# Kernel optimization log

Hardware: AMD Instinct MI355X
Metric: run time of the kernel (lower is better)

## Reference

```python
import jax, jax.numpy as jnp
import numpy as np

N, E = 20000, 320000
EPS = 1e-5
NEG_SLOPE = 0.2


def gat_conv(x, src, dst, W, att_src, att_dst, bias, num_nodes):
    # W: [Fin, H*C], att_*: [H, C], bias: [H*C]
    H, C = att_src.shape
    h = (x @ W).reshape(num_nodes, H, C)            # [N,H,C]
    a_s = jnp.einsum('nhc,hc->nh', h, att_src)      # [N,H]
    a_d = jnp.einsum('nhc,hc->nh', h, att_dst)      # [N,H]
    e = jax.nn.leaky_relu(a_s[src] + a_d[dst], NEG_SLOPE)  # [E,H]
    m = jax.ops.segment_max(e, dst, num_segments=num_nodes)       # per-dst max (self-loops guarantee non-empty)
    ex = jnp.exp(e - m[dst])
    s = jax.ops.segment_sum(ex, dst, num_segments=num_nodes)
    alpha = ex / s[dst]                              # [E,H] segment softmax
    out = jax.ops.segment_sum(h[src] * alpha[:, :, None], dst, num_segments=num_nodes)  # [N,H,C]
    return out.reshape(num_nodes, H * C) + bias


def batch_norm(x, gamma, beta):
    mu = x.mean(axis=0)
    var = x.var(axis=0)  # biased, as torch BN uses for normalization
    return (x - mu) * jax.lax.rsqrt(var + EPS) * gamma + beta


def setup_inputs() -> dict:
    key = jax.random.key(0)
    ks = jax.random.split(key, 32)
    x = jax.random.normal(ks[0], (N, 512), dtype=jnp.float32)
    edge_index = jax.random.randint(ks[1], (2, E), 0, N, dtype=jnp.int32)
    d = {"x": x, "edge_index": edge_index}
    # layer configs: (Fin, C_out, H)
    cfgs = [(512, 64, 8), (512, 64, 4), (256, 64, 2), (128, 16, 1)]
    i = 2
    for li, (fin, c, h) in enumerate(cfgs, start=1):
        sc = 1.0 / np.sqrt(fin)
        d[f"W{li}"] = jax.random.normal(ks[i], (fin, h * c), dtype=jnp.float32) * sc; i += 1
        d[f"as{li}"] = jax.random.normal(ks[i], (h, c), dtype=jnp.float32) * 0.1; i += 1
        d[f"ad{li}"] = jax.random.normal(ks[i], (h, c), dtype=jnp.float32) * 0.1; i += 1
        d[f"b{li}"] = jnp.zeros((h * c,), dtype=jnp.float32)
        if li < 4:
            d[f"g{li}"] = jnp.ones((h * c,), dtype=jnp.float32)
            d[f"be{li}"] = jnp.zeros((h * c,), dtype=jnp.float32)
    return d


def reference(x, edge_index, W1, as1, ad1, b1, g1, be1, W2, as2, ad2, b2, g2, be2, W3, as3, ad3, b3, g3, be3, W4, as4, ad4, b4):
    num_nodes = x.shape[0]
    loop = jnp.arange(num_nodes, dtype=edge_index.dtype)
    src = jnp.concatenate([edge_index[0], loop])  # add_self_loops=True
    dst = jnp.concatenate([edge_index[1], loop])
    h = gat_conv(x, src, dst, W1, as1, ad1, b1, num_nodes)
    h = jax.nn.elu(batch_norm(h, g1, be1))
    h = gat_conv(h, src, dst, W2, as2, ad2, b2, num_nodes)
    h = jax.nn.elu(batch_norm(h, g2, be2))
    h = gat_conv(h, src, dst, W3, as3, ad3, b3, num_nodes)
    h = jax.nn.elu(batch_norm(h, g3, be3))
    h = gat_conv(h, src, dst, W4, as4, ad4, b4, num_nodes)
    return jax.nn.log_softmax(h, axis=1)
```

## Files before the change

kernel.cpp:

```cpp
#include <hip/hip_runtime.h>
#include <hip/hip_bf16.h>
#include <cstdint>
#include <cstddef>

#define NN 20000
#define EE 320000
#define ET (EE + NN)
#define MPAD 20096
#define BNP 256
#define SCHUNK 20

typedef __attribute__((ext_vector_type(8))) short  short8;
typedef __attribute__((ext_vector_type(4))) float  floatx4;

__device__ inline unsigned short f2bf(float f) {
    unsigned u = __float_as_uint(f);
    u += 0x7FFFu + ((u >> 16) & 1u);
    return (unsigned short)(u >> 16);
}
__device__ inline float bf2f(unsigned short b) {
    return __uint_as_float(((unsigned)b) << 16);
}
__device__ inline float bflo(unsigned u) { return __uint_as_float(u << 16); }
__device__ inline float bfhi(unsigned u) { return __uint_as_float(u & 0xFFFF0000u); }

__global__ void zero_i32(int* __restrict__ p, int n) {
    int i = blockIdx.x * blockDim.x + threadIdx.x;
    if (i < n) p[i] = 0;
}

__global__ void cvt_a_bf16(const float* __restrict__ in, unsigned short* __restrict__ out,
                           int M, int Mpad, int K) {
    long long base = ((long long)blockIdx.x * blockDim.x + threadIdx.x) * 4;
    if (base >= (long long)Mpad * K) return;
    int row = (int)(base / K);
    float4 v = make_float4(0.f, 0.f, 0.f, 0.f);
    if (row < M) v = *(const float4*)(in + base);
    ushort4 o;
    o.x = f2bf(v.x); o.y = f2bf(v.y); o.z = f2bf(v.z); o.w = f2bf(v.w);
    *(ushort4*)(out + base) = o;
}

__global__ void cvt_w_t(const float* __restrict__ W, unsigned short* __restrict__ Wt,
                        int K, int N) {
    int i = blockIdx.x * blockDim.x + threadIdx.x;
    if (i >= K * N) return;
    int k = i / N, n = i - k * N;
    Wt[(size_t)n * K + k] = f2bf(W[i]);
}

__global__ void count_edges(const int* __restrict__ dst, int* __restrict__ cnt) {
    int e = blockIdx.x * blockDim.x + threadIdx.x;
    if (e >= ET) return;
    int d = (e < EE) ? dst[e] : (e - EE);
    atomicAdd(&cnt[d], 1);
}

__global__ __launch_bounds__(1024) void scan_fast(const int* __restrict__ cnt,
                                                  int* __restrict__ rowp,
                                                  int* __restrict__ wptr, int n) {
    __shared__ int sums[1024];
    const int t = threadIdx.x;
    const int base = t * SCHUNK;
    int local[SCHUNK];
    int acc = 0;
#pragma unroll
    for (int i = 0; i < SCHUNK; ++i) {
        int idx = base + i;
        int v = (idx < n) ? cnt[idx] : 0;
        local[i] = acc;
        acc += v;
    }
    sums[t] = acc;
    __syncthreads();
    for (int o = 1; o < 1024; o <<= 1) {
        int u = (t >= o) ? sums[t - o] : 0;
        __syncthreads();
        sums[t] += u;
        __syncthreads();
    }
    int excl = sums[t] - acc;
#pragma unroll
    for (int i = 0; i < SCHUNK; ++i) {
        int idx = base + i;
        if (idx < n) { int rp = excl + local[i]; rowp[idx] = rp; wptr[idx] = rp; }
    }
    if (t == 1023) rowp[n] = sums[1023];
}

__global__ void fill_edges(const int* __restrict__ src, const int* __restrict__ dst,
                           int* __restrict__ wptr, int* __restrict__ colx) {
    int e = blockIdx.x * blockDim.x + threadIdx.x;
    if (e >= ET) return;
    int s, d;
    if (e < EE) { s = src[e]; d = dst[e]; } else { s = e - EE; d = e - EE; }
    int pos = atomicAdd(&wptr[d], 1);
    colx[pos] = s;
}

__global__ __launch_bounds__(256) void gemm_bf16_fused(
        const unsigned short* __restrict__ A, const unsigned short* __restrict__ Bt,
        unsigned short* __restrict__ hN, float* __restrict__ aS, float* __restrict__ aD,
        const float* __restrict__ atts, const float* __restrict__ attd,
        int M, int N, int K) {
    __shared__ unsigned short As[128][40];
    __shared__ unsigned short Bs[128][40];
    const int t = threadIdx.x;
    const int lane = t & 63, wave = t >> 6;
    const int wm = wave >> 1, wn = wave & 1;
    const int quad = lane >> 4, mrow = lane & 15;
    const int row0 = blockIdx.y * 128, col0 = blockIdx.x * 128;
    const int srow = t >> 2, schunk = (t & 3) * 8;

    floatx4 acc[4][4];
#pragma unroll
    for (int i = 0; i < 4; ++i)
#pragma unroll
        for (int j = 0; j < 4; ++j)
#pragma unroll
            for (int r = 0; r < 4; ++r) acc[i][j][r] = 0.f;

    for (int k0 = 0; k0 < K; k0 += 32) {
        uint4 ra0 = *(const uint4*)(A  + (size_t)(row0 + srow)      * K + k0 + schunk);
        uint4 ra1 = *(const uint4*)(A  + (size_t)(row0 + srow + 64) * K + k0 + schunk);
        uint4 rb0 = *(const uint4*)(Bt + (size_t)(col0 + srow)      * K + k0 + schunk);
        uint4 rb1 = *(const uint4*)(Bt + (size_t)(col0 + srow + 64) * K + k0 + schunk);
        __syncthreads();
        *(uint4*)&As[srow][schunk]      = ra0;
        *(uint4*)&As[srow + 64][schunk] = ra1;
        *(uint4*)&Bs[srow][schunk]      = rb0;
        *(uint4*)&Bs[srow + 64][schunk] = rb1;
        __syncthreads();

        short8 af[4], bfr[4];
#pragma unroll
        for (int i = 0; i < 4; ++i)
            af[i] = *(const short8*)&As[wm * 64 + i * 16 + mrow][quad * 8];
#pragma unroll
        for (int j = 0; j < 4; ++j)
            bfr[j] = *(const short8*)&Bs[wn * 64 + j * 16 + mrow][quad * 8];
#pragma unroll
        for (int i = 0; i < 4; ++i)
#pragma unroll
            for (int j = 0; j < 4; ++j)
                acc[i][j] = __builtin_amdgcn_mfma_f32_16x16x32_bf16(af[i], bfr[j], acc[i][j], 0, 0, 0);
    }

    const int head = (col0 + wn * 64) >> 6;
    float attS[4], attD[4];
#pragma unroll
    for (int j = 0; j < 4; ++j) {
        attS[j] = atts[head * 64 + j * 16 + mrow];
        attD[j] = attd[head * 64 + j * 16 + mrow];
    }

#pragma unroll
    for (int i = 0; i < 4; ++i) {
#pragma unroll
        for (int r = 0; r < 4; ++r) {
            int row = row0 + wm * 64 + i * 16 + quad * 4 + r;
            float ps = acc[i][0][r] * attS[0] + acc[i][1][r] * attS[1]
                     + acc[i][2][r] * attS[2] + acc[i][3][r] * attS[3];
            float pd = acc[i][0][r] * attD[0] + acc[i][1][r] * attD[1]
                     + acc[i][2][r] * attD[2] + acc[i][3][r] * attD[3];
#pragma unroll
            for (int o = 1; o < 16; o <<= 1) {
                ps += __shfl_xor(ps, o);
                pd += __shfl_xor(pd, o);
            }
            if (row < M) {
                if (mrow == 0) {
                    aS[(size_t)head * M + row] = ps;
                    aD[(size_t)head * M + row] = pd;
                }
#pragma unroll
                for (int j = 0; j < 4; ++j)
                    hN[(size_t)row * N + col0 + wn * 64 + j * 16 + mrow] = f2bf(acc[i][j][r]);
            }
        }
    }
}

template <int HH>
__global__ __launch_bounds__(256) void gat_agg_head16(
        const unsigned short* __restrict__ hN,
        const float* __restrict__ aS, const float* __restrict__ aD,
        const int* __restrict__ rowp, const int* __restrict__ colx,
        const float* __restrict__ bias, float* __restrict__ out, int Nn) {
    constexpr int F = HH * 64;
    constexpr int G = 8 / HH;
    __shared__ uint2 pair[4][4][17];
    const int L = blockIdx.x;
    const int x8 = L & 7;
    const int hd = x8 / G;
    const int nodeblk = (L >> 3) * G + (x8 & (G - 1));
    const int wave = threadIdx.x >> 6, lane = threadIdx.x & 63;
    const int grp = lane >> 4;
    const int q   = lane & 15;
    const int n = nodeblk * 16 + wave * 4 + grp;
    if (n >= Nn) return;

    const float* aSh = aS + (size_t)hd * Nn;
    const float adv = aD[(size_t)hd * Nn + n];
    const int b0 = rowp[n], b1 = rowp[n + 1];
    const unsigned short* hbase = hN + hd * 64;

    float m = -1e30f, s = 0.f;
    float a0 = 0.f, a1 = 0.f, a2 = 0.f, a3 = 0.f;

    for (int c0 = b0; c0 < b1; c0 += 16) {
        const int cnt = min(16, b1 - c0);
        int sn = 0; float e = -1e30f;
        if (q < cnt) {
            sn = colx[c0 + q];
            float tt = aSh[sn] + adv;
            e = (tt > 0.f) ? tt : 0.2f * tt;
        }
        float mc = e;
#pragma unroll
        for (int o = 8; o > 0; o >>= 1) mc = fmaxf(mc, __shfl_xor(mc, o));
        float nm = fmaxf(m, mc);
        float sc = __expf(m - nm);
        float p = (q < cnt) ? __expf(e - nm) : 0.f;
        float ps = p;
#pragma unroll
        for (int o = 8; o > 0; o >>= 1) ps += __shfl_xor(ps, o);
        s = s * sc + ps;
        a0 *= sc; a1 *= sc; a2 *= sc; a3 *= sc;
        m = nm;

        pair[wave][grp][q] = make_uint2((unsigned)sn, __float_as_uint(p));
        __threadfence_block();

        const int iters = (cnt + 3) >> 2;
        for (int it = 0; it < iters; ++it) {
            const int j = it << 2;
            uint2 e0 = pair[wave][grp][j + 0];
            uint2 e1 = pair[wave][grp][j + 1];
            uint2 e2 = pair[wave][grp][j + 2];
            uint2 e3 = pair[wave][grp][j + 3];
            uint2 v0 = *(const uint2*)(hbase + (size_t)e0.x * F + q * 4);
            uint2 v1 = *(const uint2*)(hbase + (size_t)e1.x * F + q * 4);
            uint2 v2 = *(const uint2*)(hbase + (size_t)e2.x * F + q * 4);
            uint2 v3 = *(const uint2*)(hbase + (size_t)e3.x * F + q * 4);
            float p0 = __uint_as_float(e0.y), p1 = __uint_as_float(e1.y);
            float p2 = __uint_as_float(e2.y), p3 = __uint_as_float(e3.y);
            a0 += p0 * bflo(v0.x) + p1 * bflo(v1.x) + p2 * bflo(v2.x) + p3 * bflo(v3.x);
            a1 += p0 * bfhi(v0.x) + p1 * bfhi(v1.x) + p2 * bfhi(v2.x) + p3 * bfhi(v3.x);
            a2 += p0 * bflo(v0.y) + p1 * bflo(v1.y) + p2 * bflo(v2.y) + p3 * bflo(v3.y);
            a3 += p0 * bfhi(v0.y) + p1 * bfhi(v1.y) + p2 * bfhi(v2.y) + p3 * bfhi(v3.y);
        }
        __threadfence_block();
    }

    const float inv = 1.f / s;
    const int cb = hd * 64 + q * 4;
    float4 o4;
    o4.x = a0 * inv + bias[cb + 0];
    o4.y = a1 * inv + bias[cb + 1];
    o4.z = a2 * inv + bias[cb + 2];
    o4.w = a3 * inv + bias[cb + 3];
    *(float4*)(out + (size_t)n * F + cb) = o4;
}

__global__ __launch_bounds__(256) void gemm_l4_fused(const unsigned short* __restrict__ A,
                                                     const float* __restrict__ B,
                                                     unsigned short* __restrict__ C,
                                                     float* __restrict__ aS, float* __restrict__ aD,
                                                     const float* __restrict__ atts,
                                                     const float* __restrict__ attd,
                                                     int M, int N, int K) {
    __shared__ float As[16][65];
    __shared__ float Bs[16][64];
    const int tid = threadIdx.x;
    const int tx = tid & 15, ty = tid >> 4;
    const int row0 = blockIdx.y * 64, col0 = blockIdx.x * 64;
    const int rA = tid >> 2, kq = (tid & 3) << 2;
    const int rB = tid >> 4, cq = (tid & 15) << 2;
    float acc[4][4] = {};

    for (int k0 = 0; k0 < K; k0 += 16) {
        ushort4 ha = *(const ushort4*)(A + (size_t)(row0 + rA) * K + k0 + kq);
        float4 fb = make_float4(0.f, 0.f, 0.f, 0.f);
        int bcol = col0 + cq;
        if (bcol < N) fb = *(const float4*)(B + (size_t)(k0 + rB) * N + bcol);
        As[kq + 0][rA] = bf2f(ha.x); As[kq + 1][rA] = bf2f(ha.y);
        As[kq + 2][rA] = bf2f(ha.z); As[kq + 3][rA] = bf2f(ha.w);
        *(float4*)&Bs[rB][cq] = fb;
        __syncthreads();
#pragma unroll
        for (int k = 0; k < 16; ++k) {
            float a0 = As[k][ty * 4 + 0];
            float a1 = As[k][ty * 4 + 1];
            float a2 = As[k][ty * 4 + 2];
            float a3 = As[k][ty * 4 + 3];
            float4 b = *(float4*)&Bs[k][tx * 4];
            acc[0][0] += a0 * b.x; acc[0][1] += a0 * b.y; acc[0][2] += a0 * b.z; acc[0][3] += a0 * b.w;
            acc[1][0] += a1 * b.x; acc[1][1] += a1 * b.y; acc[1][2] += a1 * b.z; acc[1][3] += a1 * b.w;
            acc[2][0] += a2 * b.x; acc[2][1] += a2 * b.y; acc[2][2] += a2 * b.z; acc[2][3] += a2 * b.w;
            acc[3][0] += a3 * b.x; acc[3][1] += a3 * b.y; acc[3][2] += a3 * b.z; acc[3][3] += a3 * b.w;
        }
        __syncthreads();
    }
    float as_part[4], ad_part[4];
#pragma unroll
    for (int i = 0; i < 4; ++i) { as_part[i] = 0.f; ad_part[i] = 0.f; }
    if (tx < 4) {
#pragma unroll
        for (int i = 0; i < 4; ++i) {
#pragma unroll
            for (int jj = 0; jj < 4; ++jj) {
                int c = tx * 4 + jj;
                as_part[i] += acc[i][jj] * atts[c];
                ad_part[i] += acc[i][jj] * attd[c];
            }
        }
    }
#pragma unroll
    for (int i = 0; i < 4; ++i) {
        float ps = as_part[i], pd = ad_part[i];
        ps += __shfl_xor(ps, 1); ps += __shfl_xor(ps, 2);
        pd += __shfl_xor(pd, 1); pd += __shfl_xor(pd, 2);
        int r = row0 + ty * 4 + i;
        if (r < M) {
            if (tx == 0) { aS[r] = ps; aD[r] = pd; }
#pragma unroll
            for (int jj = 0; jj < 4; ++jj) {
                int c = col0 + tx * 4 + jj;
                if (c < N) C[(size_t)r * N + c] = f2bf(acc[i][jj]);
            }
        }
    }
}

template <int C>
__global__ void gat_agg_l4_ls(const unsigned short* __restrict__ ht,
                              const float* __restrict__ as, const float* __restrict__ aD,
                              const int* __restrict__ rowp, const int* __restrict__ colx,
                              const float* __restrict__ bias, float* __restrict__ out, int Nn) {
    int n = blockIdx.x * 4 + (threadIdx.x >> 6);
    int lane = threadIdx.x & 63;
    if (n >= Nn) return;
    float adv = aD[n];
    int b0 = rowp[n], b1 = rowp[n + 1];

    float m = -1e30f, s = 0.f, acc = 0.f;
    for (int c0 = b0; c0 < b1; c0 += 64) {
        int cnt = b1 - c0; if (cnt > 64) cnt = 64;
        int sn = 0; float e = -1e30f;
        if (lane < cnt) {
            sn = colx[c0 + lane];
            float tt = as[sn] + adv;
            e = (tt > 0.f) ? tt : 0.2f * tt;
        }
        float mc = e;
#pragma unroll
        for (int o = 32; o > 0; o >>= 1) mc = fmaxf(mc, __shfl_xor(mc, o));
        float nm = fmaxf(m, mc);
        float sc = __expf(m - nm);
        acc *= sc; s *= sc;
        float p = (lane < cnt) ? __expf(e - nm) : 0.f;
        float ps = p;
#pragma unroll
        for (int o = 32; o > 0; o >>= 1) ps += __shfl_xor(ps, o);
        s += ps; m = nm;

        int j = 0;
        for (; j + 4 <= cnt; j += 4) {
            int s0 = __shfl(sn, j),     s1 = __shfl(sn, j + 1);
            int s2 = __shfl(sn, j + 2), s3 = __shfl(sn, j + 3);
            float p0 = __shfl(p, j),     p1 = __shfl(p, j + 1);
            float p2 = __shfl(p, j + 2), p3 = __shfl(p, j + 3);
            float h0 = 0.f, h1 = 0.f, h2 = 0.f, h3 = 0.f;
            if (lane < C) {
                h0 = bf2f(ht[(size_t)s0 * C + lane]);
                h1 = bf2f(ht[(size_t)s1 * C + lane]);
                h2 = bf2f(ht[(size_t)s2 * C + lane]);
                h3 = bf2f(ht[(size_t)s3 * C + lane]);
            }
            acc += p0 * h0 + p1 * h1 + p2 * h2 + p3 * h3;
        }
        for (; j < cnt; ++j) {
            int sj = __shfl(sn, j);
            float pj = __shfl(p, j);
            float hv = (lane < C) ? bf2f(ht[(size_t)sj * C + lane]) : 0.f;
            acc += pj * hv;
        }
    }
    float v = (lane < C) ? (acc / s + bias[lane]) : -1e30f;
    float mx = v;
#pragma unroll
    for (int o = 8; o > 0; o >>= 1) mx = fmaxf(mx, __shfl_xor(mx, o));
    float ex = (lane < C) ? __expf(v - mx) : 0.f;
#pragma unroll
    for (int o = 8; o > 0; o >>= 1) ex += __shfl_xor(ex, o);
    float l = __logf(ex) + mx;
    if (lane < C) out[(size_t)n * C + lane] = v - l;
}

template <int F>
__global__ __launch_bounds__(256) void bn_stats_det(const float* __restrict__ x,
                                                    float* __restrict__ part,
                                                    long long total) {
    constexpr int R  = 1024 / F;
    constexpr int NT = F / 4;
    __shared__ float sd[256 * 9];
    const int t = threadIdx.x;
    long long idx = ((long long)blockIdx.x * 256 + t) * 4;
    const long long stride = (long long)gridDim.x * 1024;
    float s0 = 0, s1 = 0, s2 = 0, s3 = 0, q0 = 0, q1 = 0, q2 = 0, q3 = 0;
    for (; idx < total; idx += stride) {
        float4 v = *(const float4*)(x + idx);
        s0 += v.x; q0 += v.x * v.x;
        s1 += v.y; q1 += v.y * v.y;
        s2 += v.z; q2 += v.z * v.z;
        s3 += v.w; q3 += v.w * v.w;
    }
    sd[t * 9 + 0] = s0; sd[t * 9 + 1] = s1; sd[t * 9 + 2] = s2; sd[t * 9 + 3] = s3;
    sd[t * 9 + 4] = q0; sd[t * 9 + 5] = q1; sd[t * 9 + 6] = q2; sd[t * 9 + 7] = q3;
    __syncthreads();
    if (t < NT) {
        float a[8];
#pragma unroll
        for (int k = 0; k < 8; ++k) a[k] = sd[t * 9 + k];
        for (int r = 1; r < R; ++r)
#pragma unroll
            for (int k = 0; k < 8; ++k) a[k] += sd[(t + r * NT) * 9 + k];
        int col = t * 4;
        float* pb = part + (size_t)blockIdx.x * 2 * F;
#pragma unroll
        for (int k = 0; k < 4; ++k) {
            pb[col + k]     = a[k];
            pb[F + col + k] = a[4 + k];
        }
    }
}

template <int F>
__global__ __launch_bounds__(256) void bn_reduce_par(const float* __restrict__ part,
                                                     const float* __restrict__ gamma,
                                                     const float* __restrict__ beta,
                                                     float* __restrict__ ss,
                                                     float invN) {
    __shared__ float sd[8][33];
    const int t = threadIdx.x;
    const int pr = t >> 5;
    const int tg = t & 31;
    const int c0 = blockIdx.x * 16;
    const int col = (tg < 16) ? (c0 + tg) : (F + c0 + (tg - 16));
    float a = 0.f;
    for (int p = pr; p < BNP; p += 8)
        a += part[(size_t)p * 2 * F + col];
    sd[pr][tg] = a;
    __syncthreads();
    if (pr == 0) {
        float tot = sd[0][tg];
#pragma unroll
        for (int r = 1; r < 8; ++r) tot += sd[r][tg];
        sd[0][tg] = tot;
    }
    __syncthreads();
    if (t < 16) {
        int c = c0 + t;
        float s = sd[0][t];
        float q = sd[0][16 + t];
        float mu = s * invN;
        float var = q * invN - mu * mu;
        float sc = gamma[c] * rsqrtf(var + 1e-5f);
        ss[c] = sc;
        ss[F + c] = beta[c] - mu * sc;
    }
}

__global__ void bn_apply_elu_bf16(const float* __restrict__ x, const float* __restrict__ ss,
                                  unsigned short* __restrict__ outA,
                                  int Nn, int F, int fmask) {
    long long idx4 = ((long long)blockIdx.x * blockDim.x + threadIdx.x) * 4;
    int row = (int)(idx4 / F);
    ushort4 o = make_ushort4(0, 0, 0, 0);
    if (row < Nn) {
        int c = (int)(idx4 & fmask);
        float4 v = *(const float4*)(x + idx4);
        float v0 = v.x * ss[c + 0] + ss[F + c + 0];
        float v1 = v.y * ss[c + 1] + ss[F + c + 1];
        float v2 = v.z * ss[c + 2] + ss[F + c + 2];
        float v3 = v.w * ss[c + 3] + ss[F + c + 3];
        v0 = (v0 > 0.f) ? v0 : (__expf(v0) - 1.f);
        v1 = (v1 > 0.f) ? v1 : (__expf(v1) - 1.f);
        v2 = (v2 > 0.f) ? v2 : (__expf(v2) - 1.f);
        v3 = (v3 > 0.f) ? v3 : (__expf(v3) - 1.f);
        o.x = f2bf(v0); o.y = f2bf(v1); o.z = f2bf(v2); o.w = f2bf(v3);
    }
    *(ushort4*)(outA + idx4) = o;
}

extern "C" void kernel_launch(void* const* d_in, const int* in_sizes, int n_in,
                              void* d_out, int out_size, void* d_ws, size_t ws_size,
                              hipStream_t stream) {
    const float* x   = (const float*)d_in[0];
    const int*   ei  = (const int*)d_in[1];
    const float* W1  = (const float*)d_in[2];
    const float* as1 = (const float*)d_in[3];
    const float* ad1 = (const float*)d_in[4];
    const float* b1  = (const float*)d_in[5];
    const float* ga1 = (const float*)d_in[6];
    const float* be1 = (const float*)d_in[7];
    const float* W2  = (const float*)d_in[8];
    const float* as2 = (const float*)d_in[9];
    const float* ad2 = (const float*)d_in[10];
    const float* b2  = (const float*)d_in[11];
    const float* ga2 = (const float*)d_in[12];
    const float* be2 = (const float*)d_in[13];
    const float* W3  = (const float*)d_in[14];
    const float* as3 = (const float*)d_in[15];
    const float* ad3 = (const float*)d_in[16];
    const float* b3  = (const float*)d_in[17];
    const float* ga3 = (const float*)d_in[18];
    const float* be3 = (const float*)d_in[19];
    const float* W4  = (const float*)d_in[20];
    const float* as4 = (const float*)d_in[21];
    const float* ad4 = (const float*)d_in[22];
    const float* b4  = (const float*)d_in[23];
    float* outp = (float*)d_out;

    uint8_t* base = (uint8_t*)d_ws;
    size_t off = 0;
    auto alloc = [&](size_t nbytes) -> void* {
        off = (off + 255) & ~(size_t)255;
        void* p = base + off;
        off += nbytes;
        return p;
    };
    float* bufO = (float*)alloc((size_t)NN * 512 * 4);
    unsigned short* bufA = (unsigned short*)alloc((size_t)MPAD * 512 * 2);
    unsigned short* hN   = (unsigned short*)alloc((size_t)NN * 512 * 2);
    unsigned short* Wt1  = (unsigned short*)alloc((size_t)512 * 512 * 2);
    unsigned short* Wt2  = (unsigned short*)alloc((size_t)256 * 512 * 2);
    unsigned short* Wt3  = (unsigned short*)alloc((size_t)128 * 256 * 2);
    float* aSn  = (float*)alloc((size_t)NN * 8 * 4);
    float* aDn  = (float*)alloc((size_t)NN * 8 * 4);
    int*   cnt  = (int*)alloc((size_t)NN * 4);
    int*   rowp = (int*)alloc((size_t)(NN + 1) * 4);
    int*   wptr = (int*)alloc((size_t)NN * 4);
    int*   colx = (int*)alloc((size_t)ET * 4);
    float* bnp  = (float*)alloc((size_t)BNP * 1024 * 4);
    float* bns  = (float*)alloc((size_t)1024 * 4);

    const int* srcRow = ei;
    const int* dstRow = ei + EE;

    zero_i32<<<(NN + 255) / 256, 256, 0, stream>>>(cnt, NN);
    count_edges<<<(ET + 255) / 256, 256, 0, stream>>>(dstRow, cnt);
    scan_fast<<<1, 1024, 0, stream>>>(cnt, rowp, wptr, NN);
    fill_edges<<<(ET + 255) / 256, 256, 0, stream>>>(srcRow, dstRow, wptr, colx);

    cvt_w_t<<<(512 * 512 + 255) / 256, 256, 0, stream>>>(W1, Wt1, 512, 512);
    cvt_w_t<<<(512 * 256 + 255) / 256, 256, 0, stream>>>(W2, Wt2, 512, 256);
    cvt_w_t<<<(256 * 128 + 255) / 256, 256, 0, stream>>>(W3, Wt3, 256, 128);

    const int NBLK = (NN + 15) / 16;

    {
        cvt_a_bf16<<<((MPAD * 512 / 4) + 255) / 256, 256, 0, stream>>>(x, bufA, NN, MPAD, 512);
        dim3 g(512 / 128, MPAD / 128);
        gemm_bf16_fused<<<g, 256, 0, stream>>>(bufA, Wt1, hN, aSn, aDn, as1, ad1, NN, 512, 512);
        gat_agg_head16<8><<<NBLK * 8, 256, 0, stream>>>(hN, aSn, aDn, rowp, colx, b1, bufO, NN);
        bn_stats_det<512><<<BNP, 256, 0, stream>>>(bufO, bnp, (long long)NN * 512);
        bn_reduce_par<512><<<512 / 16, 256, 0, stream>>>(bnp, ga1, be1, bns, 1.0f / NN);
        bn_apply_elu_bf16<<<(MPAD * 512 / 4) / 256, 256, 0, stream>>>(bufO, bns, bufA, NN, 512, 511);
    }
    {
        dim3 g(256 / 128, MPAD / 128);
        gemm_bf16_fused<<<g, 256, 0, stream>>>(bufA, Wt2, hN, aSn, aDn, as2, ad2, NN, 256, 512);
        gat_agg_head16<4><<<((NBLK + 1) / 2) * 8, 256, 0, stream>>>(hN, aSn, aDn, rowp, colx, b2, bufO, NN);
        bn_stats_det<256><<<BNP, 256, 0, stream>>>(bufO, bnp, (long long)NN * 256);
        bn_reduce_par<256><<<256 / 16, 256, 0, stream>>>(bnp, ga2, be2, bns, 1.0f / NN);
        bn_apply_elu_bf16<<<(MPAD * 256 / 4) / 256, 256, 0, stream>>>(bufO, bns, bufA, NN, 256, 255);
    }
    {
        dim3 g(128 / 128, MPAD / 128);
        gemm_bf16_fused<<<g, 256, 0, stream>>>(bufA, Wt3, hN, aSn, aDn, as3, ad3, NN, 128, 256);
        gat_agg_head16<2><<<((NBLK + 3) / 4) * 8, 256, 0, stream>>>(hN, aSn, aDn, rowp, colx, b3, bufO, NN);
        bn_stats_det<128><<<BNP, 256, 0, stream>>>(bufO, bnp, (long long)NN * 128);
        bn_reduce_par<128><<<128 / 16, 256, 0, stream>>>(bnp, ga3, be3, bns, 1.0f / NN);
        bn_apply_elu_bf16<<<(MPAD * 128 / 4) / 256, 256, 0, stream>>>(bufO, bns, bufA, NN, 128, 127);
    }
    {
        dim3 g(1, (NN + 63) / 64);
        gemm_l4_fused<<<g, 256, 0, stream>>>(bufA, W4, hN, aSn, aDn, as4, ad4, NN, 16, 128);
        gat_agg_l4_ls<16><<<(NN + 3) / 4, 256, 0, stream>>>(hN, aSn, aDn, rowp, colx, b4, outp, NN);
    }
}
```

Before: 451.5 us.

## Fuse BN reduce via last-block ticket, widen aggregation chunks, merge weight casts

Folds the BN partial-sum reduction into the stats kernel: a ticket atomic lets the last block reduce all partials and write scale/shift, which removes one launch per layer. The GAT aggregation now handles 32 neighbors per chunk, with two per lane, so there are fewer online-softmax rescale rounds for typical degree around 17. The three weight-transpose launches are merged into one. In exchange, the final reduction runs serially in a single block, and it depends on the tickets being zeroed by zero_i32 on every call.

```diff
diff --git a/kernel.cpp b/kernel.cpp
--- a/kernel.cpp
+++ b/kernel.cpp
@@ -41,12 +41,20 @@
     *(ushort4*)(out + base) = o;
 }
 
-__global__ void cvt_w_t(const float* __restrict__ W, unsigned short* __restrict__ Wt,
-                        int K, int N) {
+#define W1SZ (512 * 512)
+#define W2SZ (512 * 256)
+#define W3SZ (256 * 128)
+__global__ void cvt_w_all(const float* __restrict__ W1, unsigned short* __restrict__ Wt1,
+                          const float* __restrict__ W2, unsigned short* __restrict__ Wt2,
+                          const float* __restrict__ W3, unsigned short* __restrict__ Wt3) {
     int i = blockIdx.x * blockDim.x + threadIdx.x;
-    if (i >= K * N) return;
-    int k = i / N, n = i - k * N;
-    Wt[(size_t)n * K + k] = f2bf(W[i]);
+    const float* W; unsigned short* Wt; int K, N, idx;
+    if (i < W1SZ)               { W = W1; Wt = Wt1; K = 512; N = 512; idx = i; }
+    else if (i < W1SZ + W2SZ)   { W = W2; Wt = Wt2; K = 512; N = 256; idx = i - W1SZ; }
+    else if (i < W1SZ + W2SZ + W3SZ) { W = W3; Wt = Wt3; K = 256; N = 128; idx = i - W1SZ - W2SZ; }
+    else return;
+    int k = idx / N, n = idx - k * N;
+    Wt[(size_t)n * K + k] = f2bf(W[idx]);
 }
 
 __global__ void count_edges(const int* __restrict__ dst, int* __restrict__ cnt) {
@@ -182,14 +190,14 @@
 }
 
 template <int HH>
-__global__ __launch_bounds__(256) void gat_agg_head16(
+__global__ __launch_bounds__(256) void gat_agg_head32(
         const unsigned short* __restrict__ hN,
         const float* __restrict__ aS, const float* __restrict__ aD,
         const int* __restrict__ rowp, const int* __restrict__ colx,
         const float* __restrict__ bias, float* __restrict__ out, int Nn) {
     constexpr int F = HH * 64;
     constexpr int G = 8 / HH;
-    __shared__ uint2 pair[4][4][17];
+    __shared__ uint2 pair[4][4][33];
     const int L = blockIdx.x;
     const int x8 = L & 7;
     const int hd = x8 / G;
@@ -205,52 +213,82 @@
     const int b0 = rowp[n], b1 = rowp[n + 1];
     const unsigned short* hbase = hN + hd * 64;
 
-    float m = -1e30f, s = 0.f;
+    float m, s;
     float a0 = 0.f, a1 = 0.f, a2 = 0.f, a3 = 0.f;
 
-    for (int c0 = b0; c0 < b1; c0 += 16) {
-        const int cnt = min(16, b1 - c0);
-        int sn = 0; float e = -1e30f;
-        if (q < cnt) {
-            sn = colx[c0 + q];
-            float tt = aSh[sn] + adv;
-            e = (tt > 0.f) ? tt : 0.2f * tt;
-        }
-        float mc = e;
+    auto gather = [&](int cnt) {
+        const int iters = (cnt + 3) >> 2;
+        for (int it = 0; it < iters; ++it) {
+            const int j = it << 2;
+            uint2 x0 = pair[wave][grp][j + 0];
+            uint2 x1 = pair[wave][grp][j + 1];
+            uint2 x2 = pair[wave][grp][j + 2];
+            uint2 x3 = pair[wave][grp][j + 3];
+            uint2 v0 = *(const uint2*)(hbase + (size_t)x0.x * F + q * 4);
+            uint2 v1 = *(const uint2*)(hbase + (size_t)x1.x * F + q * 4);
+            uint2 v2 = *(const uint2*)(hbase + (size_t)x2.x * F + q * 4);
+            uint2 v3 = *(const uint2*)(hbase + (size_t)x3.x * F + q * 4);
+            float p0 = __uint_as_float(x0.y), p1 = __uint_as_float(x1.y);
+            float p2 = __uint_as_float(x2.y), p3 = __uint_as_float(x3.y);
+            a0 += p0 * bflo(v0.x) + p1 * bflo(v1.x) + p2 * bflo(v2.x) + p3 * bflo(v3.x);
+            a1 += p0 * bfhi(v0.x) + p1 * bfhi(v1.x) + p2 * bfhi(v2.x) + p3 * bfhi(v3.x);
+            a2 += p0 * bflo(v0.y) + p1 * bflo(v1.y) + p2 * bflo(v2.y) + p3 * bflo(v3.y);
+            a3 += p0 * bfhi(v0.y) + p1 * bfhi(v1.y) + p2 * bfhi(v2.y) + p3 * bfhi(v3.y);
+        }
+    };
+
+    {
+        const int cnt = min(32, b1 - b0);
+        int sn0 = 0, sn1 = 0;
+        if (q < cnt)      sn0 = colx[b0 + q];
+        if (q + 16 < cnt) sn1 = colx[b0 + q + 16];
+        float t0 = aSh[sn0] + adv;
+        float t1 = aSh[sn1] + adv;
+        float e0 = (q < cnt)      ? ((t0 > 0.f) ? t0 : 0.2f * t0) : -1e30f;
+        float e1 = (q + 16 < cnt) ? ((t1 > 0.f) ? t1 : 0.2f * t1) : -1e30f;
+        float mc = fmaxf(e0, e1);
+#pragma unroll
+        for (int o = 8; o > 0; o >>= 1) mc = fmaxf(mc, __shfl_xor(mc, o));
+        m = mc;
+        float p0 = __expf(e0 - m);
+        float p1 = __expf(e1 - m);
+        float ps = p0 + p1;
+#pragma unroll
+        for (int o = 8; o > 0; o >>= 1) ps += __shfl_xor(ps, o);
+        s = ps;
+        pair[wave][grp][q]      = make_uint2((unsigned)sn0, __float_as_uint(p0));
+        pair[wave][grp][q + 16] = make_uint2((unsigned)sn1, __float_as_uint(p1));
+        __threadfence_block();
+        gather(cnt);
+    }
+
+    for (int c0 = b0 + 32; c0 < b1; c0 += 32) {
+        __threadfence_block();
+        const int cnt = min(32, b1 - c0);
+        int sn0 = 0, sn1 = 0;
+        if (q < cnt)      sn0 = colx[c0 + q];
+        if (q + 16 < cnt) sn1 = colx[c0 + q + 16];
+        float t0 = aSh[sn0] + adv;
+        float t1 = aSh[sn1] + adv;
+        float e0 = (q < cnt)      ? ((t0 > 0.f) ? t0 : 0.2f * t0) : -1e30f;
+        float e1 = (q + 16 < cnt) ? ((t1 > 0.f) ? t1 : 0.2f * t1) : -1e30f;
+        float mc = fmaxf(e0, e1);
 #pragma unroll
         for (int o = 8; o > 0; o >>= 1) mc = fmaxf(mc, __shfl_xor(mc, o));
         float nm = fmaxf(m, mc);
         float sc = __expf(m - nm);
-        float p = (q < cnt) ? __expf(e - nm) : 0.f;
-        float ps = p;
+        float p0 = __expf(e0 - nm);
+        float p1 = __expf(e1 - nm);
+        float ps = p0 + p1;
 #pragma unroll
         for (int o = 8; o > 0; o >>= 1) ps += __shfl_xor(ps, o);
         s = s * sc + ps;
         a0 *= sc; a1 *= sc; a2 *= sc; a3 *= sc;
         m = nm;
-
-        pair[wave][grp][q] = make_uint2((unsigned)sn, __float_as_uint(p));
+        pair[wave][grp][q]      = make_uint2((unsigned)sn0, __float_as_uint(p0));
+        pair[wave][grp][q + 16] = make_uint2((unsigned)sn1, __float_as_uint(p1));
         __threadfence_block();
-
-        const int iters = (cnt + 3) >> 2;
-        for (int it = 0; it < iters; ++it) {
-            const int j = it << 2;
-            uint2 e0 = pair[wave][grp][j + 0];
-            uint2 e1 = pair[wave][grp][j + 1];
-            uint2 e2 = pair[wave][grp][j + 2];
-            uint2 e3 = pair[wave][grp][j + 3];
-            uint2 v0 = *(const uint2*)(hbase + (size_t)e0.x * F + q * 4);
-            uint2 v1 = *(const uint2*)(hbase + (size_t)e1.x * F + q * 4);
-            uint2 v2 = *(const uint2*)(hbase + (size_t)e2.x * F + q * 4);
-            uint2 v3 = *(const uint2*)(hbase + (size_t)e3.x * F + q * 4);
-            float p0 = __uint_as_float(e0.y), p1 = __uint_as_float(e1.y);
-            float p2 = __uint_as_float(e2.y), p3 = __uint_as_float(e3.y);
-            a0 += p0 * bflo(v0.x) + p1 * bflo(v1.x) + p2 * bflo(v2.x) + p3 * bflo(v3.x);
-            a1 += p0 * bfhi(v0.x) + p1 * bfhi(v1.x) + p2 * bfhi(v2.x) + p3 * bfhi(v3.x);
-            a2 += p0 * bflo(v0.y) + p1 * bflo(v1.y) + p2 * bflo(v2.y) + p3 * bflo(v3.y);
-            a3 += p0 * bfhi(v0.y) + p1 * bfhi(v1.y) + p2 * bfhi(v2.y) + p3 * bfhi(v3.y);
-        }
-        __threadfence_block();
+        gather(cnt);
     }
 
     const float inv = 1.f / s;
@@ -399,9 +437,11 @@
 }
 
 template <int F>
-__global__ __launch_bounds__(256) void bn_stats_det(const float* __restrict__ x,
-                                                    float* __restrict__ part,
-                                                    long long total) {
+__global__ __launch_bounds__(256) void bn_stats_fused(
+        const float* __restrict__ x, float* __restrict__ part,
+        const float* __restrict__ gamma, const float* __restrict__ beta,
+        float* __restrict__ ss, int* __restrict__ ticket,
+        long long total, float invN) {
     constexpr int R  = 1024 / F;
     constexpr int NT = F / 4;
     __shared__ float sd[256 * 9];
@@ -434,40 +474,26 @@
             pb[F + col + k] = a[4 + k];
         }
     }
-}
-
-template <int F>
-__global__ __launch_bounds__(256) void bn_reduce_par(const float* __restrict__ part,
-                                                     const float* __restrict__ gamma,
-                                                     const float* __restrict__ beta,
-                                                     float* __restrict__ ss,
-                                                     float invN) {
-    __shared__ float sd[8][33];
-    const int t = threadIdx.x;
-    const int pr = t >> 5;
-    const int tg = t & 31;
-    const int c0 = blockIdx.x * 16;
-    const int col = (tg < 16) ? (c0 + tg) : (F + c0 + (tg - 16));
-    float a = 0.f;
-    for (int p = pr; p < BNP; p += 8)
-        a += part[(size_t)p * 2 * F + col];
-    sd[pr][tg] = a;
+    __threadfence();
+    __shared__ int amLast;
+    if (t == 0) amLast = (atomicAdd(ticket, 1) == (int)gridDim.x - 1);
     __syncthreads();
-    if (pr == 0) {
-        float tot = sd[0][tg];
-#pragma unroll
-        for (int r = 1; r < 8; ++r) tot += sd[r][tg];
-        sd[0][tg] = tot;
+    if (!amLast) return;
+    __threadfence();
+    for (int col = t; col < 2 * F; col += 256) {
+        float a = 0.f;
+        for (int p = 0; p < BNP; ++p)
+            a += part[(size_t)p * 2 * F + col];
+        sd[col] = a;
     }
     __syncthreads();
-    if (t < 16) {
-        int c = c0 + t;
-        float s = sd[0][t];
-        float q = sd[0][16 + t];
-        float mu = s * invN;
-        float var = q * invN - mu * mu;
-        float sc = gamma[c] * rsqrtf(var + 1e-5f);
-        ss[c] = sc;
+    for (int c = t; c < F; c += 256) {
+        float sum = sd[c];
+        float sq  = sd[F + c];
+        float mu  = sum * invN;
+        float var = sq * invN - mu * mu;
+        float sc  = gamma[c] * rsqrtf(var + 1e-5f);
+        ss[c]     = sc;
         ss[F + c] = beta[c] - mu * sc;
     }
 }
@@ -539,24 +565,23 @@
     unsigned short* Wt3  = (unsigned short*)alloc((size_t)128 * 256 * 2);
     float* aSn  = (float*)alloc((size_t)NN * 8 * 4);
     float* aDn  = (float*)alloc((size_t)NN * 8 * 4);
-    int*   cnt  = (int*)alloc((size_t)NN * 4);
+    int*   cnt  = (int*)alloc((size_t)(NN + 64) * 4);
     int*   rowp = (int*)alloc((size_t)(NN + 1) * 4);
     int*   wptr = (int*)alloc((size_t)NN * 4);
     int*   colx = (int*)alloc((size_t)ET * 4);
     float* bnp  = (float*)alloc((size_t)BNP * 1024 * 4);
     float* bns  = (float*)alloc((size_t)1024 * 4);
+    int* tickets = cnt + NN;
 
     const int* srcRow = ei;
     const int* dstRow = ei + EE;
 
-    zero_i32<<<(NN + 255) / 256, 256, 0, stream>>>(cnt, NN);
+    zero_i32<<<(NN + 3 + 255) / 256, 256, 0, stream>>>(cnt, NN + 3);
     count_edges<<<(ET + 255) / 256, 256, 0, stream>>>(dstRow, cnt);
     scan_fast<<<1, 1024, 0, stream>>>(cnt, rowp, wptr, NN);
     fill_edges<<<(ET + 255) / 256, 256, 0, stream>>>(srcRow, dstRow, wptr, colx);
 
-    cvt_w_t<<<(512 * 512 + 255) / 256, 256, 0, stream>>>(W1, Wt1, 512, 512);
-    cvt_w_t<<<(512 * 256 + 255) / 256, 256, 0, stream>>>(W2, Wt2, 512, 256);
-    cvt_w_t<<<(256 * 128 + 255) / 256, 256, 0, stream>>>(W3, Wt3, 256, 128);
+    cvt_w_all<<<(W1SZ + W2SZ + W3SZ) / 256, 256, 0, stream>>>(W1, Wt1, W2, Wt2, W3, Wt3);
 
     const int NBLK = (NN + 15) / 16;
 
@@ -564,25 +589,25 @@
         cvt_a_bf16<<<((MPAD * 512 / 4) + 255) / 256, 256, 0, stream>>>(x, bufA, NN, MPAD, 512);
         dim3 g(512 / 128, MPAD / 128);
         gemm_bf16_fused<<<g, 256, 0, stream>>>(bufA, Wt1, hN, aSn, aDn, as1, ad1, NN, 512, 512);
-        gat_agg_head16<8><<<NBLK * 8, 256, 0, stream>>>(hN, aSn, aDn, rowp, colx, b1, bufO, NN);
-        bn_stats_det<512><<<BNP, 256, 0, stream>>>(bufO, bnp, (long long)NN * 512);
-        bn_reduce_par<512><<<512 / 16, 256, 0, stream>>>(bnp, ga1, be1, bns, 1.0f / NN);
+        gat_agg_head32<8><<<NBLK * 8, 256, 0, stream>>>(hN, aSn, aDn, rowp, colx, b1, bufO, NN);
+        bn_stats_fused<512><<<BNP, 256, 0, stream>>>(bufO, bnp, ga1, be1, bns, tickets + 0,
+                                                     (long long)NN * 512, 1.0f / NN);
         bn_apply_elu_bf16<<<(MPAD * 512 / 4) / 256, 256, 0, stream>>>(bufO, bns, bufA, NN, 512, 511);
     }
     {
         dim3 g(256 / 128, MPAD / 128);
         gemm_bf16_fused<<<g, 256, 0, stream>>>(bufA, Wt2, hN, aSn, aDn, as2, ad2, NN, 256, 512);
-        gat_agg_head16<4><<<((NBLK + 1) / 2) * 8, 256, 0, stream>>>(hN, aSn, aDn, rowp, colx, b2, bufO, NN);
-        bn_stats_det<256><<<BNP, 256, 0, stream>>>(bufO, bnp, (long long)NN * 256);
-        bn_reduce_par<256><<<256 / 16, 256, 0, stream>>>(bnp, ga2, be2, bns, 1.0f / NN);
+        gat_agg_head32<4><<<((NBLK + 1) / 2) * 8, 256, 0, stream>>>(hN, aSn, aDn, rowp, colx, b2, bufO, NN);
+        bn_stats_fused<256><<<BNP, 256, 0, stream>>>(bufO, bnp, ga2, be2, bns, tickets + 1,
+                                                     (long long)NN * 256, 1.0f / NN);
         bn_apply_elu_bf16<<<(MPAD * 256 / 4) / 256, 256, 0, stream>>>(bufO, bns, bufA, NN, 256, 255);
     }
     {
         dim3 g(128 / 128, MPAD / 128);
         gemm_bf16_fused<<<g, 256, 0, stream>>>(bufA, Wt3, hN, aSn, aDn, as3, ad3, NN, 128, 256);
-        gat_agg_head16<2><<<((NBLK + 3) / 4) * 8, 256, 0, stream>>>(hN, aSn, aDn, rowp, colx, b3, bufO, NN);
-        bn_stats_det<128><<<BNP, 256, 0, stream>>>(bufO, bnp, (long long)NN * 128);
-        bn_reduce_par<128><<<128 / 16, 256, 0, stream>>>(bnp, ga3, be3, bns, 1.0f / NN);
+        gat_agg_head32<2><<<((NBLK + 3) / 4) * 8, 256, 0, stream>>>(hN, aSn, aDn, rowp, colx, b3, bufO, NN);
+        bn_stats_fused<128><<<BNP, 256, 0, stream>>>(bufO, bnp, ga3, be3, bns, tickets + 2,
+                                                     (long long)NN * 128, 1.0f / NN);
         bn_apply_elu_bf16<<<(MPAD * 128 / 4) / 256, 256, 0, stream>>>(bufO, bns, bufA, NN, 128, 127);
     }
     {
```

Result: slower. 533.3 us (+18.1%).
